# Optimization experiments

Measured on AMD Instinct MI355X. Metric: run time of the kernel, lower is better.

## Reference

```python
import jax, jax.numpy as jnp
import numpy as np

EPS = 1e-8
B, N, W, R = 32, 8192, 256, 4  # batch, cells, cell_width, n_reads


def setup_inputs() -> dict:
    key = jax.random.key(0)
    k1, k2, k3, k4, k5 = jax.random.split(key, 5)
    memory = jax.random.normal(k1, (B, N, W), dtype=jnp.float32)
    controls = jax.random.normal(k2, (B, 3 * W + R + 3), dtype=jnp.float32)
    read_weights = jax.random.uniform(k3, (B, R, N), dtype=jnp.float32)
    usages = jax.random.uniform(k4, (B, N), dtype=jnp.float32)
    prev_write_weights = jax.random.uniform(k5, (B, N), dtype=jnp.float32)
    return {
        "memory": memory,
        "controls": controls,
        "read_weights": read_weights,
        "usages": usages,
        "prev_write_weights": prev_write_weights,
    }


def reference(memory, controls, read_weights, usages, prev_write_weights):
    w = memory.shape[-1]
    r = read_weights.shape[1]
    b = memory.shape[0]

    # split controls per self.shapes = [W, W, W, R, 1, 1, 1]
    key_v = controls[:, :w]                                    # [B, W]
    erase_vector = jax.nn.sigmoid(controls[:, w:2 * w])        # [B, W]
    add_vector = controls[:, 2 * w:3 * w]                      # [B, W]
    p = 3 * w
    free_gates = jax.nn.sigmoid(controls[:, p:p + r])          # [B, R]
    beta = 1.0 + jax.nn.softplus(controls[:, p + r:p + r + 1])  # [B, 1]
    alloc_gate = jax.nn.sigmoid(controls[:, p + r + 1:p + r + 2])  # [B, 1]
    write_gate = jax.nn.sigmoid(controls[:, p + r + 2:p + r + 3])  # [B, 1]

    # --- usage update: phi = prod_r (1 - free_gate_r * read_weights_r) ---
    phi = jnp.prod(1.0 - free_gates[:, :, None] * read_weights, axis=1)  # [B, N]
    u = (usages + jax.lax.stop_gradient(prev_write_weights) * (1.0 - usages)) * phi  # [B, N]

    # --- allocation weighting via usage sort + cumprod + inverse scatter ---
    u_scaled = u * (1.0 - EPS) + EPS
    free_list = jnp.argsort(u_scaled, axis=-1)                     # [B, N] ascending usage
    sorted_u = jnp.take_along_axis(u_scaled, free_list, axis=-1)   # [B, N]
    u_prod = jnp.cumprod(sorted_u, axis=-1)
    one_minus = 1.0 - sorted_u
    sorted_scores = jnp.concatenate(
        [one_minus[:, :1], one_minus[:, 1:] * u_prod[:, :-1]], axis=-1)
    alloc_dist = jnp.zeros_like(sorted_scores).at[
        jnp.arange(b)[:, None], free_list].set(sorted_scores)      # [B, N]

    # --- content addressing: cosine similarity softmax ---
    dots = jnp.einsum('bnw,bw->bn', memory, key_v)                 # [B, N]
    norm = jnp.linalg.norm(key_v, axis=-1, keepdims=True) * jnp.linalg.norm(memory, axis=-1)
    content_weights = jax.nn.softmax(dots / (norm + EPS) * beta, axis=-1)  # [B, N]

    # --- gated combine ---
    write_weights = write_gate * (alloc_gate * alloc_dist +
                                  (1.0 - alloc_gate) * content_weights)   # [B, N]

    # --- memory update (dealloc=True -> erase scaled by phi) ---
    ww = write_weights[:, :, None]                                 # [B, N, 1]
    erase_matrix = (1.0 - ww * erase_vector[:, None, :]) * phi[:, :, None]
    new_memory = memory * erase_matrix + ww * add_vector[:, None, :]
    return new_memory
```

## Files before the change

kernel.cpp:

```cpp
#include <hip/hip_runtime.h>
#include <math.h>

#define BB 32
#define NN 8192
#define WW 256
#define RR 4
#define CDIM (3*WW + RR + 3)
#define EPSF 1e-8f

#define K_SEL 256
#define CAP   1024

typedef float floatx4 __attribute__((ext_vector_type(4)));

#define O_KEY    0
#define O_ERASE  (O_KEY   + BB*WW)
#define O_ADD    (O_ERASE + BB*WW)
#define O_FG     (O_ADD   + BB*WW)
#define O_KN     (O_FG    + BB*RR)
#define O_BETA   (O_KN    + BB)
#define O_AG     (O_BETA  + BB)
#define O_WG     (O_AG    + BB)
#define O_S      (O_WG    + BB)
#define O_PHI    (O_S     + BB*NN)
#define O_ALLOC  (O_PHI   + BB*NN)
#define O_USC    (O_ALLOC + BB*NN)
#define O_MX     (O_USC   + BB*NN)
#define O_IDEN   (O_MX    + BB)

__device__ __forceinline__ float sigmoidf_(float x) { return 1.0f / (1.0f + expf(-x)); }

__global__ __launch_bounds__(256) void prep_kernel(const float* __restrict__ controls,
                                                   float* __restrict__ ws) {
    int b = blockIdx.x;
    int t = threadIdx.x;
    const float* c = controls + (size_t)b * CDIM;
    float k = c[t];
    ws[O_KEY   + b*WW + t] = k;
    ws[O_ERASE + b*WW + t] = sigmoidf_(c[WW + t]);
    ws[O_ADD   + b*WW + t] = c[2*WW + t];

    __shared__ float red[256];
    red[t] = k * k;
    __syncthreads();
    for (int s = 128; s > 0; s >>= 1) {
        if (t < s) red[t] += red[t + s];
        __syncthreads();
    }
    if (t < RR) ws[O_FG + b*RR + t] = sigmoidf_(c[3*WW + t]);
    if (t == 0) {
        ws[O_KN + b] = sqrtf(red[0]);
        float x = c[3*WW + RR];
        float sp = fmaxf(x, 0.0f) + log1pf(expf(-fabsf(x)));
        ws[O_BETA + b] = 1.0f + sp;
        ws[O_AG + b] = sigmoidf_(c[3*WW + RR + 1]);
        ws[O_WG + b] = sigmoidf_(c[3*WW + RR + 2]);
    }
}

__global__ __launch_bounds__(256) void phiu_kernel(const float* __restrict__ rw,
                                                   const float* __restrict__ us,
                                                   const float* __restrict__ pw,
                                                   float* __restrict__ ws) {
    int gid = blockIdx.x * 256 + threadIdx.x;
    int b = gid >> 13;
    int n = gid & (NN - 1);
    float phi = 1.0f;
#pragma unroll
    for (int r = 0; r < RR; r++) {
        float fg = ws[O_FG + b*RR + r];
        phi *= (1.0f - fg * rw[((size_t)(b*RR + r)) * NN + n]);
    }
    float u0 = us[gid];
    float u = (u0 + pw[gid] * (1.0f - u0)) * phi;
    float usc = u * (1.0f - EPSF) + EPSF;
    ws[O_PHI   + gid] = phi;
    ws[O_USC   + gid] = usc;
    ws[O_ALLOC + gid] = 0.0f;
}

__global__ __launch_bounds__(256) void dots_kernel(const float* __restrict__ mem,
                                                   float* __restrict__ ws) {
    int b  = blockIdx.x >> 7;
    int rb = (blockIdx.x & 127) << 6;
    int wave = threadIdx.x >> 6, lane = threadIdx.x & 63;
    float4 k4 = ((const float4*)(ws + O_KEY + b*WW))[lane];
    float keynorm = ws[O_KN + b];
    float beta = ws[O_BETA + b];
#pragma unroll 4
    for (int it = 0; it < 16; ++it) {
        int n = rb + it*4 + wave;
        size_t row = (size_t)b * NN + n;
        float4 m = ((const float4*)(mem + row * WW))[lane];
        float dot = m.x*k4.x + m.y*k4.y + m.z*k4.z + m.w*k4.w;
        float nn2 = m.x*m.x + m.y*m.y + m.z*m.z + m.w*m.w;
#pragma unroll
        for (int off = 32; off > 0; off >>= 1) {
            dot += __shfl_xor(dot, off, 64);
            nn2 += __shfl_xor(nn2, off, 64);
        }
        if (lane == 0) {
            ws[O_S + row] = dot / (keynorm * sqrtf(nn2) + EPSF) * beta;
        }
    }
}

__global__ __launch_bounds__(1024) void sortalloc_kernel(float* __restrict__ ws) {
    __shared__ unsigned hist[4096];
    __shared__ unsigned long long cand[CAP];
    __shared__ unsigned uscan0[1024];
    __shared__ unsigned uscan1[1024];
    __shared__ int   selbin;
    __shared__ unsigned ccnt;

    int b = blockIdx.x, t = threadIdx.x;

    {
        const float* s = ws + O_S + (size_t)b * NN;
        float* red = (float*)uscan0;
        float mx = -INFINITY;
#pragma unroll
        for (int q = 0; q < 8; q++) mx = fmaxf(mx, s[t + q*1024]);
        red[t] = mx;
        __syncthreads();
        for (int k = 512; k > 0; k >>= 1) {
            if (t < k) red[t] = fmaxf(red[t], red[t + k]);
            __syncthreads();
        }
        mx = red[0];
        __syncthreads();
        float sum = 0.0f;
#pragma unroll
        for (int q = 0; q < 8; q++) sum += expf(s[t + q*1024] - mx);
        red[t] = sum;
        __syncthreads();
        for (int k = 512; k > 0; k >>= 1) {
            if (t < k) red[t] += red[t + k];
            __syncthreads();
        }
        if (t == 0) {
            ws[O_MX + b]   = mx;
            ws[O_IDEN + b] = 1.0f / red[0];
        }
        __syncthreads();
    }

    const float* u = ws + O_USC + (size_t)b * NN;
    for (int i = t; i < 4096; i += 1024) hist[i] = 0;
    if (t == 0) { selbin = 0x7FFFFFFF; ccnt = 0; }
    __syncthreads();

    unsigned fb[8];
#pragma unroll
    for (int q = 0; q < 8; q++) {
        fb[q] = __float_as_uint(u[t + q*1024]);
        atomicAdd(&hist[fb[q] >> 19], 1u);
    }
    __syncthreads();

    unsigned h0 = hist[4*t], h1 = hist[4*t+1], h2 = hist[4*t+2], h3 = hist[4*t+3];
    unsigned tot = h0 + h1 + h2 + h3;
    unsigned *a0 = uscan0, *a1 = uscan1;
    a0[t] = tot;
    __syncthreads();
    for (int off = 1; off < 1024; off <<= 1) {
        unsigned v = a0[t];
        if (t >= off) v += a0[t - off];
        a1[t] = v;
        __syncthreads();
        unsigned* tmp = a0; a0 = a1; a1 = tmp;
    }
    unsigned excl = (t == 0) ? 0u : a0[t - 1];
    {
        unsigned c = excl;
        unsigned hh[4] = {h0, h1, h2, h3};
#pragma unroll
        for (int j = 0; j < 4; j++) {
            c += hh[j];
            if (c >= K_SEL) { atomicMin(&selbin, 4*t + j); break; }
        }
    }
    __syncthreads();
    int Bsel = selbin;

#pragma unroll
    for (int q = 0; q < 8; q++) {
        if ((int)(fb[q] >> 19) <= Bsel) {
            unsigned pos = atomicAdd(&ccnt, 1u);
            if (pos < CAP)
                cand[pos] = (((unsigned long long)fb[q]) << 32) | (unsigned)(t + q*1024);
        }
    }
    __syncthreads();
    unsigned cnt = min(ccnt, (unsigned)CAP);
    if (t >= cnt) cand[t] = 0x3F800000FFFFFFFFull;
    __syncthreads();

    for (int k = 2; k <= CAP; k <<= 1) {
        for (int j = k >> 1; j > 0; j >>= 1) {
            int l = t ^ j;
            if (l > t) {
                unsigned long long x = cand[t], y = cand[l];
                bool asc = ((t & k) == 0);
                if ((x > y) == asc) { cand[t] = y; cand[l] = x; }
            }
            __syncthreads();
        }
    }

    float v = __uint_as_float((unsigned)(cand[t] >> 32));
    float *f0 = (float*)uscan0, *f1 = (float*)uscan1;
    f0[t] = v;
    __syncthreads();
    for (int off = 1; off < 1024; off <<= 1) {
        float x = f0[t];
        if (t >= off) x *= f0[t - off];
        f1[t] = x;
        __syncthreads();
        float* tmp = f0; f0 = f1; f1 = tmp;
    }
    float pre = (t == 0) ? 1.0f : f0[t - 1];
    unsigned idx = (unsigned)(cand[t] & 0xFFFFFFFFull);
    if (idx < NN)
        ws[O_ALLOC + (size_t)b * NN + idx] = (1.0f - v) * pre;
}

__global__ __launch_bounds__(256) void update_kernel(const float* __restrict__ mem,
                                                     const float* __restrict__ ws,
                                                     float* __restrict__ out) {
    int b  = blockIdx.x >> 7;
    int rb = (blockIdx.x & 127) << 6;
    int wave = threadIdx.x >> 6, lane = threadIdx.x & 63;
    float4 e4 = ((const float4*)(ws + O_ERASE + b*WW))[lane];
    float4 a4 = ((const float4*)(ws + O_ADD + b*WW))[lane];
    float ag = ws[O_AG + b], wg = ws[O_WG + b];
    float mx = ws[O_MX + b], iden = ws[O_IDEN + b];
#pragma unroll 4
    for (int it = 0; it < 16; ++it) {
        int n = rb + it*4 + wave;
        size_t row = (size_t)b * NN + n;
        float s   = ws[O_S + row];
        float al  = ws[O_ALLOC + row];
        float phi = ws[O_PHI + row];
        float cw  = expf(s - mx) * iden;
        float wwt = wg * (ag * al + (1.0f - ag) * cw);
        float4 m = ((const float4*)(mem + row * WW))[lane];
        floatx4 o;
        o.x = m.x * (1.0f - wwt * e4.x) * phi + wwt * a4.x;
        o.y = m.y * (1.0f - wwt * e4.y) * phi + wwt * a4.y;
        o.z = m.z * (1.0f - wwt * e4.z) * phi + wwt * a4.z;
        o.w = m.w * (1.0f - wwt * e4.w) * phi + wwt * a4.w;
        __builtin_nontemporal_store(o, &((floatx4*)(out + row * WW))[lane]);
    }
}

extern "C" void kernel_launch(void* const* d_in, const int* in_sizes, int n_in,
                              void* d_out, int out_size, void* d_ws, size_t ws_size,
                              hipStream_t stream) {
    const float* mem      = (const float*)d_in[0];
    const float* controls = (const float*)d_in[1];
    const float* rw       = (const float*)d_in[2];
    const float* us       = (const float*)d_in[3];
    const float* pw       = (const float*)d_in[4];
    float* out = (float*)d_out;
    float* ws  = (float*)d_ws;

    prep_kernel<<<BB, 256, 0, stream>>>(controls, ws);
    phiu_kernel<<<(BB * NN) / 256, 256, 0, stream>>>(rw, us, pw, ws);
    dots_kernel<<<BB * (NN / 64), 256, 0, stream>>>(mem, ws);
    sortalloc_kernel<<<BB, 1024, 0, stream>>>(ws);
    update_kernel<<<BB * (NN / 64), 256, 0, stream>>>(mem, ws, out);
}
```

Measured before the change: 168.9 us.

## Fuse softmax normalizer into dots kernel and shrink top-k sort capacity

Moves the softmax sum into the dots kernel. Because cosine similarity times beta is bounded, it stores exp(score) directly without max-subtraction and accumulates per-batch sums with atomics, so the sort kernel no longer needs its max and sum reductions. The top-k allocation kernel now runs before dots, and its bitonic sort and scan shrink from 1024 to 256 candidates, selecting 128 instead of 256. The dots kernel processes 16-lane groups per row to raise memory parallelism, and the update kernel walks blocks in reverse order, likely to reuse recently cached memory rows. The risks are a smaller candidate cap that truncates allocation weights, non-deterministic float atomics, and possible overflow without max-subtraction if beta is large.

```diff
diff --git a/kernel.cpp b/kernel.cpp
--- a/kernel.cpp
+++ b/kernel.cpp
@@ -8,8 +8,8 @@
 #define CDIM (3*WW + RR + 3)
 #define EPSF 1e-8f
 
-#define K_SEL 256
-#define CAP   1024
+#define K_SEL 128
+#define CAP   256
 
 typedef float floatx4 __attribute__((ext_vector_type(4)));
 
@@ -25,8 +25,7 @@
 #define O_PHI    (O_S     + BB*NN)
 #define O_ALLOC  (O_PHI   + BB*NN)
 #define O_USC    (O_ALLOC + BB*NN)
-#define O_MX     (O_USC   + BB*NN)
-#define O_IDEN   (O_MX    + BB)
+#define O_SUM    (O_USC   + BB*NN)
 
 __device__ __forceinline__ float sigmoidf_(float x) { return 1.0f / (1.0f + expf(-x)); }
 
@@ -55,6 +54,7 @@
         ws[O_BETA + b] = 1.0f + sp;
         ws[O_AG + b] = sigmoidf_(c[3*WW + RR + 1]);
         ws[O_WG + b] = sigmoidf_(c[3*WW + RR + 2]);
+        ws[O_SUM + b] = 0.0f;
     }
 }
 
@@ -79,73 +79,17 @@
     ws[O_ALLOC + gid] = 0.0f;
 }
 
-__global__ __launch_bounds__(256) void dots_kernel(const float* __restrict__ mem,
-                                                   float* __restrict__ ws) {
-    int b  = blockIdx.x >> 7;
-    int rb = (blockIdx.x & 127) << 6;
-    int wave = threadIdx.x >> 6, lane = threadIdx.x & 63;
-    float4 k4 = ((const float4*)(ws + O_KEY + b*WW))[lane];
-    float keynorm = ws[O_KN + b];
-    float beta = ws[O_BETA + b];
-#pragma unroll 4
-    for (int it = 0; it < 16; ++it) {
-        int n = rb + it*4 + wave;
-        size_t row = (size_t)b * NN + n;
-        float4 m = ((const float4*)(mem + row * WW))[lane];
-        float dot = m.x*k4.x + m.y*k4.y + m.z*k4.z + m.w*k4.w;
-        float nn2 = m.x*m.x + m.y*m.y + m.z*m.z + m.w*m.w;
-#pragma unroll
-        for (int off = 32; off > 0; off >>= 1) {
-            dot += __shfl_xor(dot, off, 64);
-            nn2 += __shfl_xor(nn2, off, 64);
-        }
-        if (lane == 0) {
-            ws[O_S + row] = dot / (keynorm * sqrtf(nn2) + EPSF) * beta;
-        }
-    }
-}
-
-__global__ __launch_bounds__(1024) void sortalloc_kernel(float* __restrict__ ws) {
+__global__ __launch_bounds__(1024) void topk_kernel(float* __restrict__ ws) {
     __shared__ unsigned hist[4096];
     __shared__ unsigned long long cand[CAP];
     __shared__ unsigned uscan0[1024];
     __shared__ unsigned uscan1[1024];
-    __shared__ int   selbin;
+    __shared__ int selbin;
     __shared__ unsigned ccnt;
 
     int b = blockIdx.x, t = threadIdx.x;
-
-    {
-        const float* s = ws + O_S + (size_t)b * NN;
-        float* red = (float*)uscan0;
-        float mx = -INFINITY;
-#pragma unroll
-        for (int q = 0; q < 8; q++) mx = fmaxf(mx, s[t + q*1024]);
-        red[t] = mx;
-        __syncthreads();
-        for (int k = 512; k > 0; k >>= 1) {
-            if (t < k) red[t] = fmaxf(red[t], red[t + k]);
-            __syncthreads();
-        }
-        mx = red[0];
-        __syncthreads();
-        float sum = 0.0f;
-#pragma unroll
-        for (int q = 0; q < 8; q++) sum += expf(s[t + q*1024] - mx);
-        red[t] = sum;
-        __syncthreads();
-        for (int k = 512; k > 0; k >>= 1) {
-            if (t < k) red[t] += red[t + k];
-            __syncthreads();
-        }
-        if (t == 0) {
-            ws[O_MX + b]   = mx;
-            ws[O_IDEN + b] = 1.0f / red[0];
-        }
-        __syncthreads();
-    }
-
     const float* u = ws + O_USC + (size_t)b * NN;
+
     for (int i = t; i < 4096; i += 1024) hist[i] = 0;
     if (t == 0) { selbin = 0x7FFFFFFF; ccnt = 0; }
     __syncthreads();
@@ -193,56 +137,113 @@
     }
     __syncthreads();
     unsigned cnt = min(ccnt, (unsigned)CAP);
-    if (t >= cnt) cand[t] = 0x3F800000FFFFFFFFull;
+    if (t >= cnt && t < CAP) cand[t] = 0x3F800000FFFFFFFFull;
     __syncthreads();
 
     for (int k = 2; k <= CAP; k <<= 1) {
         for (int j = k >> 1; j > 0; j >>= 1) {
-            int l = t ^ j;
-            if (l > t) {
-                unsigned long long x = cand[t], y = cand[l];
-                bool asc = ((t & k) == 0);
-                if ((x > y) == asc) { cand[t] = y; cand[l] = x; }
+            if (t < CAP) {
+                int l = t ^ j;
+                if (l > t) {
+                    unsigned long long x = cand[t], y = cand[l];
+                    bool asc = ((t & k) == 0);
+                    if ((x > y) == asc) { cand[t] = y; cand[l] = x; }
+                }
             }
             __syncthreads();
         }
     }
 
-    float v = __uint_as_float((unsigned)(cand[t] >> 32));
+    float v = 1.0f;
+    if (t < CAP) v = __uint_as_float((unsigned)(cand[t] >> 32));
     float *f0 = (float*)uscan0, *f1 = (float*)uscan1;
-    f0[t] = v;
-    __syncthreads();
-    for (int off = 1; off < 1024; off <<= 1) {
-        float x = f0[t];
-        if (t >= off) x *= f0[t - off];
-        f1[t] = x;
+    if (t < CAP) f0[t] = v;
+    __syncthreads();
+    for (int off = 1; off < CAP; off <<= 1) {
+        float x = 0.0f;
+        if (t < CAP) { x = f0[t]; if (t >= off) x *= f0[t - off]; }
+        __syncthreads();
+        if (t < CAP) f1[t] = x;
         __syncthreads();
         float* tmp = f0; f0 = f1; f1 = tmp;
     }
-    float pre = (t == 0) ? 1.0f : f0[t - 1];
-    unsigned idx = (unsigned)(cand[t] & 0xFFFFFFFFull);
-    if (idx < NN)
-        ws[O_ALLOC + (size_t)b * NN + idx] = (1.0f - v) * pre;
+    if (t < CAP) {
+        float pre = (t == 0) ? 1.0f : f0[t - 1];
+        unsigned idx = (unsigned)(cand[t] & 0xFFFFFFFFull);
+        if (idx < NN)
+            ws[O_ALLOC + (size_t)b * NN + idx] = (1.0f - v) * pre;
+    }
+}
+
+__global__ __launch_bounds__(256) void dots_kernel(const float* __restrict__ mem,
+                                                   float* __restrict__ ws) {
+    int b  = blockIdx.x >> 7;
+    int rb = (blockIdx.x & 127) << 6;
+    int wave = threadIdx.x >> 6;
+    int lane = threadIdx.x & 63;
+    int g  = lane >> 4;
+    int li = lane & 15;
+
+    float4 k4[4];
+#pragma unroll
+    for (int k = 0; k < 4; k++)
+        k4[k] = ((const float4*)(ws + O_KEY + b*WW))[li + k*16];
+    float kn   = ws[O_KN + b];
+    float beta = ws[O_BETA + b];
+
+    float psum = 0.0f;
+#pragma unroll
+    for (int p = 0; p < 4; p++) {
+        int n = rb + wave*16 + p*4 + g;
+        const float4* mrow = (const float4*)(mem + ((size_t)b * NN + n) * WW);
+        float dot = 0.0f, nn2 = 0.0f;
+#pragma unroll
+        for (int k = 0; k < 4; k++) {
+            float4 m = mrow[li + k*16];
+            dot += m.x*k4[k].x + m.y*k4[k].y + m.z*k4[k].z + m.w*k4[k].w;
+            nn2 += m.x*m.x + m.y*m.y + m.z*m.z + m.w*m.w;
+        }
+#pragma unroll
+        for (int off = 8; off > 0; off >>= 1) {
+            dot += __shfl_xor(dot, off, 64);
+            nn2 += __shfl_xor(nn2, off, 64);
+        }
+        if (li == 0) {
+            float pv = expf(dot / (kn * sqrtf(nn2) + EPSF) * beta);
+            ws[O_S + (size_t)b * NN + n] = pv;
+            psum += pv;
+        }
+    }
+    __shared__ float red[16];
+    if (li == 0) red[wave*4 + g] = psum;
+    __syncthreads();
+    if (threadIdx.x == 0) {
+        float s = 0.0f;
+#pragma unroll
+        for (int i = 0; i < 16; i++) s += red[i];
+        atomicAdd(&ws[O_SUM + b], s);
+    }
 }
 
 __global__ __launch_bounds__(256) void update_kernel(const float* __restrict__ mem,
                                                      const float* __restrict__ ws,
                                                      float* __restrict__ out) {
-    int b  = blockIdx.x >> 7;
-    int rb = (blockIdx.x & 127) << 6;
+    int bid = gridDim.x - 1 - blockIdx.x;
+    int b  = bid >> 7;
+    int rb = (bid & 127) << 6;
     int wave = threadIdx.x >> 6, lane = threadIdx.x & 63;
     float4 e4 = ((const float4*)(ws + O_ERASE + b*WW))[lane];
     float4 a4 = ((const float4*)(ws + O_ADD + b*WW))[lane];
     float ag = ws[O_AG + b], wg = ws[O_WG + b];
-    float mx = ws[O_MX + b], iden = ws[O_IDEN + b];
+    float iden = 1.0f / ws[O_SUM + b];
 #pragma unroll 4
     for (int it = 0; it < 16; ++it) {
         int n = rb + it*4 + wave;
         size_t row = (size_t)b * NN + n;
-        float s   = ws[O_S + row];
+        float pv  = ws[O_S + row];
         float al  = ws[O_ALLOC + row];
         float phi = ws[O_PHI + row];
-        float cw  = expf(s - mx) * iden;
+        float cw  = pv * iden;
         float wwt = wg * (ag * al + (1.0f - ag) * cw);
         float4 m = ((const float4*)(mem + row * WW))[lane];
         floatx4 o;
@@ -267,7 +268,7 @@
 
     prep_kernel<<<BB, 256, 0, stream>>>(controls, ws);
     phiu_kernel<<<(BB * NN) / 256, 256, 0, stream>>>(rw, us, pw, ws);
+    topk_kernel<<<BB, 1024, 0, stream>>>(ws);
     dots_kernel<<<BB * (NN / 64), 256, 0, stream>>>(mem, ws);
-    sortalloc_kernel<<<BB, 1024, 0, stream>>>(ws);
     update_kernel<<<BB * (NN / 64), 256, 0, stream>>>(mem, ws, out);
 }
```

Result: no change. 169.3 us (+0.2%).
